# Performance work log

Hardware: AMD Instinct MI355X
Metric: run time of the kernel (lower is better)

## Reference

```python
import jax, jax.numpy as jnp
import numpy as np

K, D = 512, 64

def setup_inputs() -> dict:
    key = jax.random.key(0)
    k1, k2 = jax.random.split(key)
    z_e_x = jax.random.normal(k1, (64, D, 64, 64), dtype=jnp.float32)  # [B, D, H, W]
    # nn.Embedding weight init: uniform(-1/K, 1/K)
    emb = jax.random.uniform(k2, (K, D), dtype=jnp.float32, minval=-1.0 / K, maxval=1.0 / K)
    return {"z_e_x": z_e_x, "emb": emb}

def reference(z_e_x, emb):
    # Squared L2 distance expanded: ||z||^2 - 2 z.e + ||e||^2, avoiding the
    # [B, K, D, H, W] broadcast intermediate of the original torch code.
    z_sq = jnp.sum(z_e_x * z_e_x, axis=1)              # [B, H, W]
    e_sq = jnp.sum(emb * emb, axis=1)                  # [K]
    cross = jnp.einsum('bdhw,kd->bkhw', z_e_x, emb)    # [B, K, H, W]
    dists = z_sq[:, None] - 2.0 * cross + e_sq[None, :, None, None]
    latents = jnp.argmin(dists, axis=1)                # [B, H, W] int
    return latents
```

## Files before the change

### kernel.cpp

```cpp
#include <hip/hip_runtime.h>

#define KCODES 512
#define DDIM 64

typedef __attribute__((ext_vector_type(8))) short bf16x8;
typedef __attribute__((ext_vector_type(4))) float f32x4;

__device__ __forceinline__ void bf16_split(float v, unsigned short& hi, unsigned short& lo) {
    unsigned u = __float_as_uint(v);
    unsigned r = u + 0x7fffu + ((u >> 16) & 1u);
    hi = (unsigned short)(r >> 16);
    float hf = __uint_as_float(((unsigned)hi) << 16);
    float l = v - hf;
    unsigned u2 = __float_as_uint(l);
    unsigned r2 = u2 + 0x7fffu + ((u2 >> 16) & 1u);
    lo = (unsigned short)(r2 >> 16);
}

__device__ __forceinline__ float np_dist_strided(const float* __restrict__ zp,
                                                 const float* __restrict__ e, float esqk) {
    float zq = 0.f, cr = 0.f;
    #pragma unroll 8
    for (int d = 0; d < DDIM; ++d) {
        float zv = zp[(size_t)d * 4096];
        zq = __fadd_rn(zq, __fmul_rn(zv, zv));
        cr = __fadd_rn(cr, __fmul_rn(zv, e[d]));
    }
    return __fadd_rn(__fsub_rn(zq, __fmul_rn(2.0f, cr)), esqk);
}

__global__ __launch_bounds__(256) void vq_argmin_kernel(
    const float* __restrict__ z, const float* __restrict__ emb, int* __restrict__ out)
{
    __shared__ unsigned short ehi[128 * 64];
    __shared__ unsigned short elo[128 * 64];
    __shared__ float esq[KCODES];

    const int t    = threadIdx.x;
    const int lane = t & 63;
    const int w    = t >> 6;
    const int g    = lane >> 4;
    const int p16  = lane & 15;

    for (int k = t; k < KCODES; k += 256) {
        const float* e = emb + k * DDIM;
        float r[8];
        #pragma unroll
        for (int j = 0; j < 8; ++j) r[j] = __fmul_rn(e[j], e[j]);
        #pragma unroll
        for (int i = 8; i < DDIM; i += 8)
            #pragma unroll
            for (int j = 0; j < 8; ++j)
                r[j] = __fadd_rn(r[j], __fmul_rn(e[i + j], e[i + j]));
        esq[k] = __fadd_rn(
            __fadd_rn(__fadd_rn(r[0], r[1]), __fadd_rn(r[2], r[3])),
            __fadd_rn(__fadd_rn(r[4], r[5]), __fadd_rn(r[6], r[7])));
    }

    const int P0  = blockIdx.x * 256;
    const int bb  = P0 >> 12;
    const int hwW = (P0 & 4095) + w * 64;
    const float* zbase = z + (size_t)bb * (DDIM * 4096);

    bf16x8 zh[4][2], zl[4][2];
    float  sab[4];
    #pragma unroll
    for (int s = 0; s < 4; ++s) {
        sab[s] = 0.f;
        #pragma unroll
        for (int c = 0; c < 2; ++c) {
            #pragma unroll
            for (int j = 0; j < 8; ++j) {
                int d = g * 8 + j + c * 32;
                float v = zbase[(size_t)d * 4096 + hwW + s * 16 + p16];
                sab[s] += fabsf(v);
                unsigned short h, l;
                bf16_split(v, h, l);
                zh[s][c][j] = (short)h;
                zl[s][c][j] = (short)l;
            }
        }
    }

    float m1[4], m2[4], m3[4];
    int   i1[4], i2[4];
    #pragma unroll
    for (int s = 0; s < 4; ++s) { m1[s] = m2[s] = m3[s] = 3.0e38f; i1[s] = i2[s] = 0; }

    const int rx  = p16 & 7;
    const int jj0 = (g) ^ rx;
    const int jj1 = (4 + g) ^ rx;
    const int g4  = g * 4;

    for (int pp = 0; pp < 4; ++pp) {
        __syncthreads();
        {
            const int r  = t >> 1;
            const int dh = (t & 1) * 32;
            const float* src = emb + (pp * 128 + r) * DDIM + dh;
            #pragma unroll
            for (int q = 0; q < 4; ++q) {
                bf16x8 hh, ll;
                #pragma unroll
                for (int j = 0; j < 8; ++j) {
                    unsigned short h, l;
                    bf16_split(src[q * 8 + j], h, l);
                    hh[j] = (short)h; ll[j] = (short)l;
                }
                int jidx = (dh >> 3) + q;
                int idx  = r * 64 + ((jidx ^ (r & 7)) << 3);
                *(bf16x8*)&ehi[idx] = hh;
                *(bf16x8*)&elo[idx] = ll;
            }
        }
        __syncthreads();

        #pragma unroll
        for (int tt = 0; tt < 8; ++tt) {
            const int rowbase = tt * 16 + p16;
            const int ib0 = rowbase * 64 + jj0 * 8;
            const int ib1 = rowbase * 64 + jj1 * 8;
            bf16x8 ah0 = *(const bf16x8*)&ehi[ib0];
            bf16x8 ah1 = *(const bf16x8*)&ehi[ib1];
            bf16x8 al0 = *(const bf16x8*)&elo[ib0];
            bf16x8 al1 = *(const bf16x8*)&elo[ib1];
            const float* eq = &esq[pp * 128 + tt * 16 + g4];
            float e0 = eq[0], e1 = eq[1], e2 = eq[2], e3 = eq[3];
            const int cb = pp * 128 + tt * 16;

            #pragma unroll
            for (int s = 0; s < 4; ++s) {
                f32x4 acc = {0.f, 0.f, 0.f, 0.f};
                acc = __builtin_amdgcn_mfma_f32_16x16x32_bf16(ah0, zh[s][0], acc, 0, 0, 0);
                acc = __builtin_amdgcn_mfma_f32_16x16x32_bf16(ah1, zh[s][1], acc, 0, 0, 0);
                acc = __builtin_amdgcn_mfma_f32_16x16x32_bf16(al0, zh[s][0], acc, 0, 0, 0);
                acc = __builtin_amdgcn_mfma_f32_16x16x32_bf16(al1, zh[s][1], acc, 0, 0, 0);
                acc = __builtin_amdgcn_mfma_f32_16x16x32_bf16(ah0, zl[s][0], acc, 0, 0, 0);
                acc = __builtin_amdgcn_mfma_f32_16x16x32_bf16(ah1, zl[s][1], acc, 0, 0, 0);
                #pragma unroll
                for (int r = 0; r < 4; ++r) {
                    float er = (r == 0) ? e0 : (r == 1) ? e1 : (r == 2) ? e2 : e3;
                    float sc = fmaf(-2.0f, acc[r], er);
                    int   cd = cb + g4 + r;
                    bool b1 = sc < m1[s];
                    bool b2 = sc < m2[s];
                    m3[s] = b2 ? m2[s] : fminf(m3[s], sc);
                    m2[s] = b1 ? m1[s] : fminf(m2[s], sc);
                    i2[s] = b1 ? i1[s] : (b2 ? cd : i2[s]);
                    m1[s] = fminf(m1[s], sc);
                    i1[s] = b1 ? cd : i1[s];
                }
            }
        }
    }

    #pragma unroll
    for (int s = 0; s < 4; ++s) {
        #pragma unroll
        for (int st = 0; st < 2; ++st) {
            int mask = 16 << st;
            float om1 = __shfl_xor(m1[s], mask); int oi1 = __shfl_xor(i1[s], mask);
            float om2 = __shfl_xor(m2[s], mask); int oi2 = __shfl_xor(i2[s], mask);
            float om3 = __shfl_xor(m3[s], mask);
            float osa = __shfl_xor(sab[s], mask);
            sab[s] += osa;
            bool  take1 = om1 < m1[s];
            float hi  = take1 ? m1[s] : om1;  int hii = take1 ? i1[s] : oi1;
            float n1  = take1 ? om1 : m1[s];  int ni1 = take1 ? oi1 : i1[s];
            float mn2 = fminf(m2[s], om2);    int mi2 = (om2 < m2[s]) ? oi2 : i2[s];
            bool  sec = hi < mn2;
            float n2  = sec ? hi : mn2;       int ni2 = sec ? hii : mi2;
            float n3  = fminf(fmaxf(hi, mn2), fminf(m3[s], om3));
            m1[s] = n1; i1[s] = ni1; m2[s] = n2; i2[s] = ni2; m3[s] = n3;
        }
    }

    float M1v = (g == 0) ? m1[0] : (g == 1) ? m1[1] : (g == 2) ? m1[2] : m1[3];
    float M2v = (g == 0) ? m2[0] : (g == 1) ? m2[1] : (g == 2) ? m2[2] : m2[3];
    float M3v = (g == 0) ? m3[0] : (g == 1) ? m3[1] : (g == 2) ? m3[2] : m3[3];
    float SA  = (g == 0) ? sab[0] : (g == 1) ? sab[1] : (g == 2) ? sab[2] : sab[3];
    int   I1  = (g == 0) ? i1[0] : (g == 1) ? i1[1] : (g == 2) ? i1[2] : i1[3];
    int   I2  = (g == 0) ? i2[0] : (g == 1) ? i2[1] : (g == 2) ? i2[2] : i2[3];

    const float MARG = SA * 2.0e-7f + 2.5e-5f;
    const bool  f2 = (M2v - M1v) < MARG;
    const bool  f3 = (M3v - M1v) < MARG;

    const float* zrow = zbase + hwW + lane;
    int idx = I1;

    if (f2 && !f3) {
        int a = min(I1, I2), b = max(I1, I2);
        float Da = np_dist_strided(zrow, emb + a * DDIM, esq[a]);
        float Db = np_dist_strided(zrow, emb + b * DDIM, esq[b]);
        idx = (Db < Da) ? b : a;
    }

    unsigned long long bal = __ballot(f3);
    while (bal) {
        int pix = __ffsll((long long)bal) - 1;
        bal &= bal - 1;
        const float* zf = zbase + hwW + pix;
        float bD = 3.0e38f; int bC = 0;
        #pragma unroll
        for (int j = 0; j < 8; ++j) {
            int c = j * 64 + lane;
            float D = np_dist_strided(zf, emb + c * DDIM, esq[c]);
            if (D < bD) { bD = D; bC = c; }
        }
        #pragma unroll
        for (int mk = 1; mk < 64; mk <<= 1) {
            float oD = __shfl_xor(bD, mk);
            int   oC = __shfl_xor(bC, mk);
            if (oD < bD || (oD == bD && oC < bC)) { bD = oD; bC = oC; }
        }
        if (lane == pix) idx = bC;
    }

    out[P0 + w * 64 + lane] = idx;
}

extern "C" void kernel_launch(void* const* d_in, const int* in_sizes, int n_in,
                              void* d_out, int out_size, void* d_ws, size_t ws_size,
                              hipStream_t stream)
{
    const float* z   = (const float*)d_in[0];
    const float* emb = (const float*)d_in[1];
    int* out = (int*)d_out;
    dim3 grid(out_size / 256), block(256);
    hipLaunchKernelGGL(vq_argmin_kernel, grid, block, 0, stream, z, emb, out);
}
```

Before: 117.8 us.

## Precompute bf16 codebook image in prekernel, double-buffer LDS, pack top-3 keys

A one-block prekernel computes the codebook squared norms, a split bf16 hi/lo swizzled image, and the max absolute codebook value into workspace. The main kernel then streams this image into double-buffered shared memory with register staging, so per-block conversion and half of the barriers go away. The top-3 tracking packs the quantized score and code index into one unsigned key so integer min/max can be used. The fallback-triggering margins are rescaled using the codebook max. It adds an extra launch and a workspace dependency, plus a fallback kernel for when the workspace is too small.

Result: slower. 147.1 us (+24.9%).

```diff
diff --git a/kernel.cpp b/kernel.cpp
--- a/kernel.cpp
+++ b/kernel.cpp
@@ -5,6 +5,15 @@
 
 typedef __attribute__((ext_vector_type(8))) short bf16x8;
 typedef __attribute__((ext_vector_type(4))) float f32x4;
+
+#define WS_IMG    0
+#define WS_ESQB   131072
+#define WS_ESQ    133120
+#define WS_MAXE   135168
+#define WS_NEEDED 135172
+
+__device__ __forceinline__ unsigned umin_(unsigned a, unsigned b) { return a < b ? a : b; }
+__device__ __forceinline__ unsigned umax_(unsigned a, unsigned b) { return a > b ? a : b; }
 
 __device__ __forceinline__ void bf16_split(float v, unsigned short& hi, unsigned short& lo) {
     unsigned u = __float_as_uint(v);
@@ -29,12 +38,65 @@
     return __fadd_rn(__fsub_rn(zq, __fmul_rn(2.0f, cr)), esqk);
 }
 
-__global__ __launch_bounds__(256) void vq_argmin_kernel(
-    const float* __restrict__ z, const float* __restrict__ emb, int* __restrict__ out)
-{
-    __shared__ unsigned short ehi[128 * 64];
-    __shared__ unsigned short elo[128 * 64];
-    __shared__ float esq[KCODES];
+__global__ __launch_bounds__(512) void vq_pre_kernel(const float* __restrict__ emb,
+                                                     char* __restrict__ ws)
+{
+    __shared__ float wmax[8];
+    const int k = threadIdx.x;
+    const float* e = emb + k * DDIM;
+
+    float r[8];
+    #pragma unroll
+    for (int j = 0; j < 8; ++j) r[j] = __fmul_rn(e[j], e[j]);
+    #pragma unroll
+    for (int i = 8; i < DDIM; i += 8)
+        #pragma unroll
+        for (int j = 0; j < 8; ++j)
+            r[j] = __fadd_rn(r[j], __fmul_rn(e[i + j], e[i + j]));
+    float esq = __fadd_rn(
+        __fadd_rn(__fadd_rn(r[0], r[1]), __fadd_rn(r[2], r[3])),
+        __fadd_rn(__fadd_rn(r[4], r[5]), __fadd_rn(r[6], r[7])));
+    ((float*)(ws + WS_ESQ))[k]  = esq;
+    ((float*)(ws + WS_ESQB))[k] = __fadd_rn(esq, 0.5f);
+
+    const int pass = k >> 6, rr = k & 63;
+    unsigned short* ehi = (unsigned short*)(ws + WS_IMG + pass * 16384);
+    unsigned short* elo = (unsigned short*)(ws + WS_IMG + pass * 16384 + 8192);
+    float me = 0.f;
+    #pragma unroll
+    for (int jidx = 0; jidx < 8; ++jidx) {
+        bf16x8 hh, ll;
+        #pragma unroll
+        for (int j = 0; j < 8; ++j) {
+            float v = e[jidx * 8 + j];
+            me = fmaxf(me, fabsf(v));
+            unsigned short h, l;
+            bf16_split(v, h, l);
+            hh[j] = (short)h; ll[j] = (short)l;
+        }
+        int off = rr * 64 + ((jidx ^ (rr & 7)) << 3);
+        *(bf16x8*)&ehi[off] = hh;
+        *(bf16x8*)&elo[off] = ll;
+    }
+
+    #pragma unroll
+    for (int m = 1; m < 64; m <<= 1) me = fmaxf(me, __shfl_xor(me, m));
+    if ((k & 63) == 0) wmax[k >> 6] = me;
+    __syncthreads();
+    if (k == 0) {
+        float M = wmax[0];
+        #pragma unroll
+        for (int i = 1; i < 8; ++i) M = fmaxf(M, wmax[i]);
+        *(float*)(ws + WS_MAXE) = M;
+    }
+}
+
+__global__ __launch_bounds__(256) void vq_main_kernel(
+    const float* __restrict__ z, const float* __restrict__ emb,
+    const char* __restrict__ ws, int* __restrict__ out)
+{
+    __shared__ __align__(16) unsigned short buf[2][8192];
+    __shared__ __align__(16) float esqb[KCODES];
 
     const int t    = threadIdx.x;
     const int lane = t & 63;
@@ -42,20 +104,9 @@
     const int g    = lane >> 4;
     const int p16  = lane & 15;
 
-    for (int k = t; k < KCODES; k += 256) {
-        const float* e = emb + k * DDIM;
-        float r[8];
-        #pragma unroll
-        for (int j = 0; j < 8; ++j) r[j] = __fmul_rn(e[j], e[j]);
-        #pragma unroll
-        for (int i = 8; i < DDIM; i += 8)
-            #pragma unroll
-            for (int j = 0; j < 8; ++j)
-                r[j] = __fadd_rn(r[j], __fmul_rn(e[i + j], e[i + j]));
-        esq[k] = __fadd_rn(
-            __fadd_rn(__fadd_rn(r[0], r[1]), __fadd_rn(r[2], r[3])),
-            __fadd_rn(__fadd_rn(r[4], r[5]), __fadd_rn(r[6], r[7])));
-    }
+    esqb[t]       = ((const float*)(ws + WS_ESQB))[t];
+    esqb[t + 256] = ((const float*)(ws + WS_ESQB))[t + 256];
+    const float maxe = *((const float*)(ws + WS_MAXE));
 
     const int P0  = blockIdx.x * 256;
     const int bb  = P0 >> 12;
@@ -82,51 +133,42 @@
         }
     }
 
-    float m1[4], m2[4], m3[4];
-    int   i1[4], i2[4];
-    #pragma unroll
-    for (int s = 0; s < 4; ++s) { m1[s] = m2[s] = m3[s] = 3.0e38f; i1[s] = i2[s] = 0; }
-
-    const int rx  = p16 & 7;
-    const int jj0 = (g) ^ rx;
-    const int jj1 = (4 + g) ^ rx;
+    const float4* img = (const float4*)(ws + WS_IMG);
+    float4 st0, st1, st2, st3;
+#define ISSUE(P)  { int b_ = (P) * 1024 + t; st0 = img[b_]; st1 = img[b_ + 256]; \
+                    st2 = img[b_ + 512]; st3 = img[b_ + 768]; }
+#define WRITEB(BI){ float4* dst_ = (float4*)&buf[BI][0]; dst_[t] = st0; dst_[t + 256] = st1; \
+                    dst_[t + 512] = st2; dst_[t + 768] = st3; }
+
+    ISSUE(0);
+    WRITEB(0);
+    ISSUE(1);
+    __syncthreads();
+
+    unsigned m1[4], m2[4], m3[4];
+    #pragma unroll
+    for (int s = 0; s < 4; ++s) { m1[s] = m2[s] = m3[s] = 0xFFFFFFFFu; }
+
+    const int jj0 = g ^ (p16 & 7);
+    const int jj1 = (4 + g) ^ (p16 & 7);
     const int g4  = g * 4;
 
-    for (int pp = 0; pp < 4; ++pp) {
-        __syncthreads();
-        {
-            const int r  = t >> 1;
-            const int dh = (t & 1) * 32;
-            const float* src = emb + (pp * 128 + r) * DDIM + dh;
-            #pragma unroll
-            for (int q = 0; q < 4; ++q) {
-                bf16x8 hh, ll;
-                #pragma unroll
-                for (int j = 0; j < 8; ++j) {
-                    unsigned short h, l;
-                    bf16_split(src[q * 8 + j], h, l);
-                    hh[j] = (short)h; ll[j] = (short)l;
-                }
-                int jidx = (dh >> 3) + q;
-                int idx  = r * 64 + ((jidx ^ (r & 7)) << 3);
-                *(bf16x8*)&ehi[idx] = hh;
-                *(bf16x8*)&elo[idx] = ll;
-            }
-        }
-        __syncthreads();
-
-        #pragma unroll
-        for (int tt = 0; tt < 8; ++tt) {
-            const int rowbase = tt * 16 + p16;
-            const int ib0 = rowbase * 64 + jj0 * 8;
-            const int ib1 = rowbase * 64 + jj1 * 8;
+    for (int pp = 0; pp < 8; ++pp) {
+        const unsigned short* ehi = &buf[pp & 1][0];
+        const unsigned short* elo = &buf[pp & 1][4096];
+
+        #pragma unroll
+        for (int tt = 0; tt < 4; ++tt) {
+            const int row = tt * 16 + p16;
+            const int ib0 = row * 64 + (jj0 << 3);
+            const int ib1 = row * 64 + (jj1 << 3);
             bf16x8 ah0 = *(const bf16x8*)&ehi[ib0];
             bf16x8 ah1 = *(const bf16x8*)&ehi[ib1];
             bf16x8 al0 = *(const bf16x8*)&elo[ib0];
             bf16x8 al1 = *(const bf16x8*)&elo[ib1];
-            const float* eq = &esq[pp * 128 + tt * 16 + g4];
-            float e0 = eq[0], e1 = eq[1], e2 = eq[2], e3 = eq[3];
-            const int cb = pp * 128 + tt * 16;
+            const int ct = pp * 64 + tt * 16;
+            f32x4 eq = *(const f32x4*)&esqb[ct + g4];
+            const unsigned c0 = (unsigned)(ct + g4);
 
             #pragma unroll
             for (int s = 0; s < 4; ++s) {
@@ -138,61 +180,66 @@
                 acc = __builtin_amdgcn_mfma_f32_16x16x32_bf16(ah0, zl[s][0], acc, 0, 0, 0);
                 acc = __builtin_amdgcn_mfma_f32_16x16x32_bf16(ah1, zl[s][1], acc, 0, 0, 0);
                 #pragma unroll
-                for (int r = 0; r < 4; ++r) {
-                    float er = (r == 0) ? e0 : (r == 1) ? e1 : (r == 2) ? e2 : e3;
-                    float sc = fmaf(-2.0f, acc[r], er);
-                    int   cd = cb + g4 + r;
-                    bool b1 = sc < m1[s];
-                    bool b2 = sc < m2[s];
-                    m3[s] = b2 ? m2[s] : fminf(m3[s], sc);
-                    m2[s] = b1 ? m1[s] : fminf(m2[s], sc);
-                    i2[s] = b1 ? i1[s] : (b2 ? cd : i2[s]);
-                    m1[s] = fminf(m1[s], sc);
-                    i1[s] = b1 ? cd : i1[s];
+                for (int rr = 0; rr < 4; ++rr) {
+                    float sc = fmaf(-2.f, acc[rr], eq[rr]);
+                    unsigned key = (__float_as_uint(sc) & 0xFFFFFE00u) | (c0 + (unsigned)rr);
+                    unsigned big  = umax_(key, m1[s]);
+                    m1[s]         = umin_(key, m1[s]);
+                    unsigned big2 = umax_(big, m2[s]);
+                    m2[s]         = umin_(big, m2[s]);
+                    m3[s]         = umin_(big2, m3[s]);
                 }
             }
         }
+
+        if (pp < 7) {
+            WRITEB((pp + 1) & 1);
+            if (pp < 6) ISSUE(pp + 2);
+        }
+        __syncthreads();
     }
 
     #pragma unroll
     for (int s = 0; s < 4; ++s) {
         #pragma unroll
-        for (int st = 0; st < 2; ++st) {
-            int mask = 16 << st;
-            float om1 = __shfl_xor(m1[s], mask); int oi1 = __shfl_xor(i1[s], mask);
-            float om2 = __shfl_xor(m2[s], mask); int oi2 = __shfl_xor(i2[s], mask);
-            float om3 = __shfl_xor(m3[s], mask);
-            float osa = __shfl_xor(sab[s], mask);
+        for (int st2 = 0; st2 < 2; ++st2) {
+            const int mk = 16 << st2;
+            unsigned b1 = (unsigned)__shfl_xor((int)m1[s], mk);
+            unsigned b2 = (unsigned)__shfl_xor((int)m2[s], mk);
+            unsigned b3 = (unsigned)__shfl_xor((int)m3[s], mk);
+            float osa = __shfl_xor(sab[s], mk);
             sab[s] += osa;
-            bool  take1 = om1 < m1[s];
-            float hi  = take1 ? m1[s] : om1;  int hii = take1 ? i1[s] : oi1;
-            float n1  = take1 ? om1 : m1[s];  int ni1 = take1 ? oi1 : i1[s];
-            float mn2 = fminf(m2[s], om2);    int mi2 = (om2 < m2[s]) ? oi2 : i2[s];
-            bool  sec = hi < mn2;
-            float n2  = sec ? hi : mn2;       int ni2 = sec ? hii : mi2;
-            float n3  = fminf(fmaxf(hi, mn2), fminf(m3[s], om3));
-            m1[s] = n1; i1[s] = ni1; m2[s] = n2; i2[s] = ni2; m3[s] = n3;
-        }
-    }
-
-    float M1v = (g == 0) ? m1[0] : (g == 1) ? m1[1] : (g == 2) ? m1[2] : m1[3];
-    float M2v = (g == 0) ? m2[0] : (g == 1) ? m2[1] : (g == 2) ? m2[2] : m2[3];
-    float M3v = (g == 0) ? m3[0] : (g == 1) ? m3[1] : (g == 2) ? m3[2] : m3[3];
-    float SA  = (g == 0) ? sab[0] : (g == 1) ? sab[1] : (g == 2) ? sab[2] : sab[3];
-    int   I1  = (g == 0) ? i1[0] : (g == 1) ? i1[1] : (g == 2) ? i1[2] : i1[3];
-    int   I2  = (g == 0) ? i2[0] : (g == 1) ? i2[1] : (g == 2) ? i2[2] : i2[3];
-
-    const float MARG = SA * 2.0e-7f + 2.5e-5f;
-    const bool  f2 = (M2v - M1v) < MARG;
-    const bool  f3 = (M3v - M1v) < MARG;
+            unsigned M1 = umin_(m1[s], b1), x = umax_(m1[s], b1);
+            unsigned c  = umin_(m2[s], b2), d = umax_(m2[s], b2);
+            unsigned M2 = umin_(x, c),      e2 = umax_(x, c);
+            unsigned M3 = umin_(umin_(e2, d), umin_(m3[s], b3));
+            m1[s] = M1; m2[s] = M2; m3[s] = M3;
+        }
+    }
+
+    unsigned K1 = (g == 0) ? m1[0] : (g == 1) ? m1[1] : (g == 2) ? m1[2] : m1[3];
+    unsigned K2 = (g == 0) ? m2[0] : (g == 1) ? m2[1] : (g == 2) ? m2[2] : m2[3];
+    unsigned K3 = (g == 0) ? m3[0] : (g == 1) ? m3[1] : (g == 2) ? m3[2] : m3[3];
+    float    SA = (g == 0) ? sab[0] : (g == 1) ? sab[1] : (g == 2) ? sab[2] : sab[3];
+
+    const float qs1 = __uint_as_float(K1 & 0xFFFFFE00u);
+    const float qs2 = __uint_as_float(K2 & 0xFFFFFE00u);
+    const float qs3 = __uint_as_float(K3 & 0xFFFFFE00u);
+    const int   I1  = (int)(K1 & 511u);
+    const int   I2  = (int)(K2 & 511u);
+
+    const float MARG = 1.0e-4f + 3.0e-5f * (SA * maxe);
+    const bool  f2 = (qs2 - qs1) < MARG;
+    const bool  f3 = ((qs3 - qs1) < MARG) || (2.f * SA * maxe > 0.45f) || !(qs1 > 0.f);
 
     const float* zrow = zbase + hwW + lane;
+    const float* esqr = (const float*)(ws + WS_ESQ);
     int idx = I1;
 
     if (f2 && !f3) {
         int a = min(I1, I2), b = max(I1, I2);
-        float Da = np_dist_strided(zrow, emb + a * DDIM, esq[a]);
-        float Db = np_dist_strided(zrow, emb + b * DDIM, esq[b]);
+        float Da = np_dist_strided(zrow, emb + a * DDIM, esqr[a]);
+        float Db = np_dist_strided(zrow, emb + b * DDIM, esqr[b]);
         idx = (Db < Da) ? b : a;
     }
 
@@ -205,7 +252,7 @@
         #pragma unroll
         for (int j = 0; j < 8; ++j) {
             int c = j * 64 + lane;
-            float D = np_dist_strided(zf, emb + c * DDIM, esq[c]);
+            float D = np_dist_strided(zf, emb + c * DDIM, esqr[c]);
             if (D < bD) { bD = D; bC = c; }
         }
         #pragma unroll
@@ -218,6 +265,101 @@
     }
 
     out[P0 + w * 64 + lane] = idx;
+#undef ISSUE
+#undef WRITEB
+}
+
+__device__ __forceinline__ float fb_fast_score(const float4* __restrict__ e4,
+                                               const float* zr, float esqk)
+{
+    float a0 = 0.f, a1 = 0.f, a2 = 0.f, a3 = 0.f;
+    #pragma unroll
+    for (int i = 0; i < DDIM / 4; ++i) {
+        float4 v = e4[i];
+        a0 = fmaf(zr[4*i+0], v.x, a0);
+        a1 = fmaf(zr[4*i+1], v.y, a1);
+        a2 = fmaf(zr[4*i+2], v.z, a2);
+        a3 = fmaf(zr[4*i+3], v.w, a3);
+    }
+    return fmaf(-2.f, (a0 + a1) + (a2 + a3), esqk);
+}
+
+__device__ __forceinline__ float fb_np_dist(const float* __restrict__ e,
+                                            const float* zr, float zsq, float esqk)
+{
+    float c = 0.f;
+    #pragma unroll
+    for (int d = 0; d < DDIM; ++d)
+        c = __fadd_rn(c, __fmul_rn(zr[d], e[d]));
+    return __fadd_rn(__fsub_rn(zsq, __fmul_rn(2.0f, c)), esqk);
+}
+
+__global__ __launch_bounds__(256) void vq_fallback_kernel(
+    const float* __restrict__ z, const float* __restrict__ emb, int* __restrict__ out)
+{
+    __shared__ float esq[KCODES];
+    const int t = threadIdx.x;
+    for (int k = t; k < KCODES; k += 256) {
+        const float* e = emb + k * DDIM;
+        float r[8];
+        #pragma unroll
+        for (int j = 0; j < 8; ++j) r[j] = __fmul_rn(e[j], e[j]);
+        #pragma unroll
+        for (int i = 8; i < DDIM; i += 8)
+            #pragma unroll
+            for (int j = 0; j < 8; ++j)
+                r[j] = __fadd_rn(r[j], __fmul_rn(e[i+j], e[i+j]));
+        esq[k] = __fadd_rn(
+            __fadd_rn(__fadd_rn(r[0], r[1]), __fadd_rn(r[2], r[3])),
+            __fadd_rn(__fadd_rn(r[4], r[5]), __fadd_rn(r[6], r[7])));
+    }
+    __syncthreads();
+    const int p  = blockIdx.x * 256 + t;
+    const int b  = p >> 12;
+    const int hw = p & 4095;
+    const float* zp = z + (size_t)b * (DDIM * 4096) + hw;
+    float zr[DDIM];
+    #pragma unroll
+    for (int d = 0; d < DDIM; ++d) zr[d] = zp[(size_t)d * 4096];
+    float zsq = __fmul_rn(zr[0], zr[0]);
+    #pragma unroll
+    for (int d = 1; d < DDIM; ++d)
+        zsq = __fadd_rn(zsq, __fmul_rn(zr[d], zr[d]));
+    float m1 = 3.0e38f, m2 = 3.0e38f, m3 = 3.0e38f;
+    int   i1 = 0, i2 = 0;
+    for (int k = 0; k < KCODES; ++k) {
+        const float s = fb_fast_score(reinterpret_cast<const float4*>(emb + k * DDIM), zr, esq[k]);
+        const bool b1 = s < m1, b2 = s < m2, b3 = s < m3;
+        const float nm3 = b2 ? m2 : (b3 ? s : m3);
+        const float nm2 = b1 ? m1 : (b2 ? s : m2);
+        const int   ni2 = b1 ? i1 : (b2 ? k : i2);
+        const float nm1 = b1 ? s : m1;
+        const int   ni1 = b1 ? k : i1;
+        m3 = nm3; m2 = nm2; i2 = ni2; m1 = nm1; i1 = ni1;
+    }
+    int idx = i1;
+    if (m2 - m1 < 6.0e-5f) {
+        if (m3 - m1 >= 6.0e-5f) {
+            const float D1 = fb_np_dist(emb + i1 * DDIM, zr, zsq, esq[i1]);
+            const float D2 = fb_np_dist(emb + i2 * DDIM, zr, zsq, esq[i2]);
+            const int   ka = (i1 < i2) ? i1 : i2;
+            const int   kb = (i1 < i2) ? i2 : i1;
+            const float Da = (i1 < i2) ? D1 : D2;
+            const float Db = (i1 < i2) ? D2 : D1;
+            idx = (Db < Da) ? kb : ka;
+        } else {
+            float bestD = 3.0e38f; int bi = 0; bool found = false;
+            for (int k = 0; k < KCODES; ++k) {
+                const float s = fb_fast_score(reinterpret_cast<const float4*>(emb + k * DDIM), zr, esq[k]);
+                if (s < m1 + 6.0e-5f) {
+                    const float Dk = fb_np_dist(emb + k * DDIM, zr, zsq, esq[k]);
+                    if (!found || Dk < bestD) { bestD = Dk; bi = k; found = true; }
+                }
+            }
+            idx = bi;
+        }
+    }
+    out[p] = idx;
 }
 
 extern "C" void kernel_launch(void* const* d_in, const int* in_sizes, int n_in,
@@ -227,6 +369,12 @@
     const float* z   = (const float*)d_in[0];
     const float* emb = (const float*)d_in[1];
     int* out = (int*)d_out;
-    dim3 grid(out_size / 256), block(256);
-    hipLaunchKernelGGL(vq_argmin_kernel, grid, block, 0, stream, z, emb, out);
-}
+    if (ws_size >= (size_t)WS_NEEDED) {
+        hipLaunchKernelGGL(vq_pre_kernel, dim3(1), dim3(512), 0, stream, emb, (char*)d_ws);
+        hipLaunchKernelGGL(vq_main_kernel, dim3(out_size / 256), dim3(256), 0, stream,
+                           z, emb, (const char*)d_ws, out);
+    } else {
+        hipLaunchKernelGGL(vq_fallback_kernel, dim3(out_size / 256), dim3(256), 0, stream,
+                           z, emb, out);
+    }
+}
```
